# Optimization experiments

Measured on AMD Instinct MI355X. Metric: run time of the kernel, lower is better.

## Reference

```python
import jax, jax.numpy as jnp
import numpy as np

N_NODES, N_EDGES, N_INC = 50000, 10000, 800000
IN_C, HID_C, OUT_C = 128, 128, 128
EPS = 1e-5  # BatchNorm1d default


def setup_inputs() -> dict:
    key = jax.random.key(0)
    ks = jax.random.split(key, 6)
    x = jax.random.normal(ks[0], (N_NODES, IN_C), jnp.float32)
    node_idx = jax.random.randint(ks[1], (N_INC,), 0, N_NODES)
    edge_idx = jax.random.randint(ks[2], (N_INC,), 0, N_EDGES)
    hyperedge_index = jnp.stack([node_idx, edge_idx])  # [2, nnz]
    hyperedge_weight = jnp.ones((N_EDGES,), jnp.float32)
    s1 = 1.0 / np.sqrt(IN_C)
    s2 = 1.0 / np.sqrt(HID_C)
    W1 = jax.random.uniform(ks[3], (HID_C, IN_C), jnp.float32, -s1, s1)
    b1 = jnp.zeros((HID_C,), jnp.float32)
    gamma = jnp.ones((HID_C,), jnp.float32)
    beta = jnp.zeros((HID_C,), jnp.float32)
    W2 = jax.random.uniform(ks[4], (OUT_C, HID_C), jnp.float32, -s2, s2)
    b2 = jnp.zeros((OUT_C,), jnp.float32)
    return dict(x=x, hyperedge_index=hyperedge_index, hyperedge_weight=hyperedge_weight,
                W1=W1, b1=b1, gamma=gamma, beta=beta, W2=W2, b2=b2)


def _hconv(x, W, b, node_idx, edge_idx, hw):
    """PyG HypergraphConv (heads=1, no attention): D^-1 H B^-1 H^T (X W^T) + b."""
    x = x @ W.T  # [N, out_c]; lin has bias=False in PyG
    # node degrees weighted by hyperedge weight
    D = jax.ops.segment_sum(hw[edge_idx], node_idx, num_segments=N_NODES)
    Dinv = jnp.where(D > 0, 1.0 / D, 0.0)
    # hyperedge degrees
    Bdeg = jax.ops.segment_sum(jnp.ones_like(edge_idx, dtype=x.dtype), edge_idx,
                               num_segments=N_EDGES)
    Binv = jnp.where(Bdeg > 0, 1.0 / Bdeg, 0.0)
    # node -> hyperedge: e_e = B_e^-1 * sum_{i in e} x_i
    e = jax.ops.segment_sum(Binv[edge_idx][:, None] * x[node_idx], edge_idx,
                            num_segments=N_EDGES)
    # hyperedge -> node: out_i = D_i^-1 * sum_{e ni i} e_e
    out = jax.ops.segment_sum(Dinv[node_idx][:, None] * e[edge_idx], node_idx,
                              num_segments=N_NODES)
    return out + b  # PyG adds bias after propagation


def reference(x, hyperedge_index, hyperedge_weight, W1, b1, gamma, beta, W2, b2):
    node_idx, edge_idx = hyperedge_index[0], hyperedge_index[1]
    h = _hconv(x, W1, b1, node_idx, edge_idx, hyperedge_weight)
    # BatchNorm1d (training mode: batch statistics, biased variance)
    mu = h.mean(axis=0)
    var = h.var(axis=0)
    h = gamma * (h - mu) * jax.lax.rsqrt(var + EPS) + beta
    return _hconv(h, W2, b2, node_idx, edge_idx, hyperedge_weight)
```

## Files before the change

### kernel.cpp

```cpp
#include <hip/hip_runtime.h>

#define NN 50000
#define NE 10000
#define NI 800000
#define CH 128
#define EPSV 1e-5f
#define ESTR 160
#define NSTR 64
#define NPART 8
#define FCHUNK 2000
#define EPB 8

__global__ __launch_bounds__(256) void k_fill_part(const int* __restrict__ nidx,
    const int* __restrict__ eidx, int* __restrict__ cnt_e,
    int* __restrict__ cnt_n, unsigned short* __restrict__ ell_e,
    unsigned short* __restrict__ ell_n) {
  const int part = blockIdx.x & (NPART - 1);
  const int i0 = (blockIdx.x >> 3) * FCHUNK;
  const int e_lo = part * (NE / NPART), e_hi = e_lo + NE / NPART;
  const int n_lo = part * (NN / NPART), n_hi = n_lo + NN / NPART;
  for (int i = i0 + threadIdx.x; i < i0 + FCHUNK; i += 256) {
    int n = nidx[i], e = eidx[i];
    if (e >= e_lo && e < e_hi) {
      int ce = atomicAdd(&cnt_e[e], 1);
      if (ce < ESTR) ell_e[(long)e * ESTR + ce] = (unsigned short)n;
    }
    if (n >= n_lo && n < n_hi) {
      int cn = atomicAdd(&cnt_n[n], 1);
      if (cn < NSTR) ell_n[(long)n * NSTR + cn] = (unsigned short)e;
    }
  }
}

__global__ __launch_bounds__(256) void k_edge_gemm(const int* __restrict__ cnt_e,
    const unsigned short* __restrict__ ell_e, const float* __restrict__ X,
    const float* __restrict__ W, float* __restrict__ Eout,
    const float* __restrict__ scale, const float* __restrict__ shift) {
  __shared__ float As[EPB][132];
  const int tid = threadIdx.x;
  const int e0 = blockIdx.x * EPB;
  const int lane = tid & 31, grp = tid >> 5;
  const int c = lane * 4;

  const int e = e0 + grp;
  int t = (e < NE) ? cnt_e[e] : 0;
  if (t > ESTR) t = ESTR;
  const unsigned short* base = ell_e + (long)e * ESTR;
  float4 acc = make_float4(0.f, 0.f, 0.f, 0.f);
  int j = 0;
  for (; j + 8 <= t; j += 8) {
    ushort4 na = *reinterpret_cast<const ushort4*>(base + j);
    ushort4 nb = *reinterpret_cast<const ushort4*>(base + j + 4);
    float4 v0 = *reinterpret_cast<const float4*>(&X[(long)na.x * CH + c]);
    float4 v1 = *reinterpret_cast<const float4*>(&X[(long)na.y * CH + c]);
    float4 v2 = *reinterpret_cast<const float4*>(&X[(long)na.z * CH + c]);
    float4 v3 = *reinterpret_cast<const float4*>(&X[(long)na.w * CH + c]);
    float4 v4 = *reinterpret_cast<const float4*>(&X[(long)nb.x * CH + c]);
    float4 v5 = *reinterpret_cast<const float4*>(&X[(long)nb.y * CH + c]);
    float4 v6 = *reinterpret_cast<const float4*>(&X[(long)nb.z * CH + c]);
    float4 v7 = *reinterpret_cast<const float4*>(&X[(long)nb.w * CH + c]);
    acc.x += ((v0.x + v1.x) + (v2.x + v3.x)) + ((v4.x + v5.x) + (v6.x + v7.x));
    acc.y += ((v0.y + v1.y) + (v2.y + v3.y)) + ((v4.y + v5.y) + (v6.y + v7.y));
    acc.z += ((v0.z + v1.z) + (v2.z + v3.z)) + ((v4.z + v5.z) + (v6.z + v7.z));
    acc.w += ((v0.w + v1.w) + (v2.w + v3.w)) + ((v4.w + v5.w) + (v6.w + v7.w));
  }
  for (; j + 4 <= t; j += 4) {
    ushort4 na = *reinterpret_cast<const ushort4*>(base + j);
    float4 v0 = *reinterpret_cast<const float4*>(&X[(long)na.x * CH + c]);
    float4 v1 = *reinterpret_cast<const float4*>(&X[(long)na.y * CH + c]);
    float4 v2 = *reinterpret_cast<const float4*>(&X[(long)na.z * CH + c]);
    float4 v3 = *reinterpret_cast<const float4*>(&X[(long)na.w * CH + c]);
    acc.x += (v0.x + v1.x) + (v2.x + v3.x);
    acc.y += (v0.y + v1.y) + (v2.y + v3.y);
    acc.z += (v0.z + v1.z) + (v2.z + v3.z);
    acc.w += (v0.w + v1.w) + (v2.w + v3.w);
  }
  for (; j < t; ++j) {
    int n = base[j];
    float4 v = *reinterpret_cast<const float4*>(&X[(long)n * CH + c]);
    acc.x += v.x; acc.y += v.y; acc.z += v.z; acc.w += v.w;
  }
  float binv = (t > 0) ? 1.f / (float)t : 0.f;
  float4 m = make_float4(acc.x * binv, acc.y * binv, acc.z * binv, acc.w * binv);
  if (scale) {
    m.x = scale[c + 0] * m.x + shift[c + 0];
    m.y = scale[c + 1] * m.y + shift[c + 1];
    m.z = scale[c + 2] * m.z + shift[c + 2];
    m.w = scale[c + 3] * m.w + shift[c + 3];
  }
  As[grp][c + 0] = m.x; As[grp][c + 1] = m.y;
  As[grp][c + 2] = m.z; As[grp][c + 3] = m.w;
  __syncthreads();

  float a0 = 0.f, a1 = 0.f, a2 = 0.f, a3 = 0.f;
  #pragma unroll 4
  for (int kq = 0; kq < 32; ++kq) {
    float4 a = *reinterpret_cast<const float4*>(&As[grp][kq * 4]);
    float4 w0 = *reinterpret_cast<const float4*>(&W[(long)(c + 0) * CH + kq * 4]);
    float4 w1 = *reinterpret_cast<const float4*>(&W[(long)(c + 1) * CH + kq * 4]);
    float4 w2 = *reinterpret_cast<const float4*>(&W[(long)(c + 2) * CH + kq * 4]);
    float4 w3 = *reinterpret_cast<const float4*>(&W[(long)(c + 3) * CH + kq * 4]);
    a0 += a.x * w0.x + a.y * w0.y + a.z * w0.z + a.w * w0.w;
    a1 += a.x * w1.x + a.y * w1.y + a.z * w1.z + a.w * w1.w;
    a2 += a.x * w2.x + a.y * w2.y + a.z * w2.z + a.w * w2.w;
    a3 += a.x * w3.x + a.y * w3.y + a.z * w3.z + a.w * w3.w;
  }
  if (e < NE) {
    float4 o = make_float4(a0, a1, a2, a3);
    *reinterpret_cast<float4*>(&Eout[(long)e * CH + c]) = o;
  }
}

__global__ __launch_bounds__(256) void k_gather_node(const int* __restrict__ cnt_n,
    const unsigned short* __restrict__ ell_n, const float* __restrict__ hw,
    const float* __restrict__ Eacc, const float* __restrict__ bias,
    float* __restrict__ Out) {
  int gid = blockIdx.x * 256 + threadIdx.x;
  int i = gid >> 5;
  if (i >= NN) return;
  int c = (gid & 31) * 4;
  const float4 bb = *reinterpret_cast<const float4*>(&bias[c]);
  int t = cnt_n[i];
  if (t > NSTR) t = NSTR;
  const unsigned short* base = ell_n + (long)i * NSTR;
  float4 acc = make_float4(0.f, 0.f, 0.f, 0.f);
  float wsum = 0.f;
  int j = 0;
  for (; j + 8 <= t; j += 8) {
    ushort4 ea = *reinterpret_cast<const ushort4*>(base + j);
    ushort4 eb = *reinterpret_cast<const ushort4*>(base + j + 4);
    wsum += ((hw[ea.x] + hw[ea.y]) + (hw[ea.z] + hw[ea.w])) +
            ((hw[eb.x] + hw[eb.y]) + (hw[eb.z] + hw[eb.w]));
    float4 v0 = *reinterpret_cast<const float4*>(&Eacc[(long)ea.x * CH + c]);
    float4 v1 = *reinterpret_cast<const float4*>(&Eacc[(long)ea.y * CH + c]);
    float4 v2 = *reinterpret_cast<const float4*>(&Eacc[(long)ea.z * CH + c]);
    float4 v3 = *reinterpret_cast<const float4*>(&Eacc[(long)ea.w * CH + c]);
    float4 v4 = *reinterpret_cast<const float4*>(&Eacc[(long)eb.x * CH + c]);
    float4 v5 = *reinterpret_cast<const float4*>(&Eacc[(long)eb.y * CH + c]);
    float4 v6 = *reinterpret_cast<const float4*>(&Eacc[(long)eb.z * CH + c]);
    float4 v7 = *reinterpret_cast<const float4*>(&Eacc[(long)eb.w * CH + c]);
    acc.x += ((v0.x + v1.x) + (v2.x + v3.x)) + ((v4.x + v5.x) + (v6.x + v7.x));
    acc.y += ((v0.y + v1.y) + (v2.y + v3.y)) + ((v4.y + v5.y) + (v6.y + v7.y));
    acc.z += ((v0.z + v1.z) + (v2.z + v3.z)) + ((v4.z + v5.z) + (v6.z + v7.z));
    acc.w += ((v0.w + v1.w) + (v2.w + v3.w)) + ((v4.w + v5.w) + (v6.w + v7.w));
  }
  for (; j + 4 <= t; j += 4) {
    ushort4 ea = *reinterpret_cast<const ushort4*>(base + j);
    wsum += (hw[ea.x] + hw[ea.y]) + (hw[ea.z] + hw[ea.w]);
    float4 v0 = *reinterpret_cast<const float4*>(&Eacc[(long)ea.x * CH + c]);
    float4 v1 = *reinterpret_cast<const float4*>(&Eacc[(long)ea.y * CH + c]);
    float4 v2 = *reinterpret_cast<const float4*>(&Eacc[(long)ea.z * CH + c]);
    float4 v3 = *reinterpret_cast<const float4*>(&Eacc[(long)ea.w * CH + c]);
    acc.x += (v0.x + v1.x) + (v2.x + v3.x);
    acc.y += (v0.y + v1.y) + (v2.y + v3.y);
    acc.z += (v0.z + v1.z) + (v2.z + v3.z);
    acc.w += (v0.w + v1.w) + (v2.w + v3.w);
  }
  for (; j < t; ++j) {
    int ee = base[j];
    wsum += hw[ee];
    float4 v = *reinterpret_cast<const float4*>(&Eacc[(long)ee * CH + c]);
    acc.x += v.x; acc.y += v.y; acc.z += v.z; acc.w += v.w;
  }
  float dinv = wsum > 0.f ? 1.f / wsum : 0.f;
  float4 o;
  o.x = dinv * acc.x + bb.x; o.y = dinv * acc.y + bb.y;
  o.z = dinv * acc.z + bb.z; o.w = dinv * acc.w + bb.w;
  *reinterpret_cast<float4*>(&Out[(long)i * CH + c]) = o;
}

__global__ __launch_bounds__(256) void k_colstats(const float* __restrict__ H,
    float* __restrict__ colsum, float* __restrict__ colsq) {
  const int tid = threadIdx.x;
  const int cp = (tid & 63) * 2;
  const int rh = tid >> 6;
  float s0 = 0, s1 = 0, q0 = 0, q1 = 0;
  for (int r = blockIdx.x * 4 + rh; r < NN; r += gridDim.x * 4) {
    float2 v = *reinterpret_cast<const float2*>(&H[(long)r * CH + cp]);
    s0 += v.x; s1 += v.y; q0 += v.x * v.x; q1 += v.y * v.y;
  }
  __shared__ float sh[256][4];
  sh[tid][0] = s0; sh[tid][1] = s1; sh[tid][2] = q0; sh[tid][3] = q1;
  __syncthreads();
  if (tid < 64) {
    float ts0 = 0, ts1 = 0, tq0 = 0, tq1 = 0;
    #pragma unroll
    for (int g = 0; g < 4; ++g) {
      ts0 += sh[tid + g * 64][0]; ts1 += sh[tid + g * 64][1];
      tq0 += sh[tid + g * 64][2]; tq1 += sh[tid + g * 64][3];
    }
    atomicAdd(&colsum[cp], ts0); atomicAdd(&colsum[cp + 1], ts1);
    atomicAdd(&colsq[cp], tq0);  atomicAdd(&colsq[cp + 1], tq1);
  }
}

__global__ void k_bn_params(const float* __restrict__ colsum,
    const float* __restrict__ colsq, const float* __restrict__ gamma,
    const float* __restrict__ beta, float* __restrict__ scl,
    float* __restrict__ shf) {
  int c = threadIdx.x;
  if (c >= CH) return;
  float mu = colsum[c] * (1.f / NN);
  float var = colsq[c] * (1.f / NN) - mu * mu;
  float a = gamma[c] * rsqrtf(var + EPSV);
  scl[c] = a;
  shf[c] = beta[c] - mu * a;
}

extern "C" void kernel_launch(void* const* d_in, const int* in_sizes, int n_in,
                              void* d_out, int out_size, void* d_ws, size_t ws_size,
                              hipStream_t stream) {
  const float* x     = (const float*)d_in[0];
  const int*   hidx  = (const int*)d_in[1];
  const float* hw    = (const float*)d_in[2];
  const float* W1    = (const float*)d_in[3];
  const float* b1    = (const float*)d_in[4];
  const float* gamma = (const float*)d_in[5];
  const float* beta  = (const float*)d_in[6];
  const float* W2    = (const float*)d_in[7];
  const float* b2    = (const float*)d_in[8];
  float* out = (float*)d_out;

  const int* nidx = hidx;
  const int* eidx = hidx + NI;

  char* wb = (char*)d_ws;
  int* cnt_e = (int*)wb;
  int* cnt_n = cnt_e + NE;
  unsigned short* ell_e = (unsigned short*)(cnt_n + NN);
  unsigned short* ell_n = ell_e + (long)NE * ESTR;
  size_t bytes = (size_t)(NE + NN) * 4 + ((size_t)NE * ESTR + (size_t)NN * NSTR) * 2;
  bytes = (bytes + 15) & ~(size_t)15;
  float* wf = (float*)(wb + bytes);
  float* colsum = wf;
  float* colsq  = wf + 128;
  float* scl    = wf + 256;
  float* shf    = wf + 384;
  float* Eacc   = wf + 512;
  float* H      = out;

  hipMemsetAsync(cnt_e, 0, (size_t)(NE + NN) * sizeof(int), stream);
  hipMemsetAsync(colsum, 0, 256 * sizeof(float), stream);
  k_fill_part<<<(NI / FCHUNK) * NPART, 256, 0, stream>>>(nidx, eidx, cnt_e, cnt_n,
                                                         ell_e, ell_n);

  k_edge_gemm<<<NE / EPB, 256, 0, stream>>>(cnt_e, ell_e, x, W1, Eacc,
                                            nullptr, nullptr);
  k_gather_node<<<(NN * 32 + 255) / 256, 256, 0, stream>>>(cnt_n, ell_n, hw,
                                                           Eacc, b1, H);
  k_colstats<<<512, 256, 0, stream>>>(H, colsum, colsq);
  k_bn_params<<<1, 128, 0, stream>>>(colsum, colsq, gamma, beta, scl, shf);

  k_edge_gemm<<<NE / EPB, 256, 0, stream>>>(cnt_e, ell_e, H, W2, Eacc,
                                            scl, shf);
  k_gather_node<<<(NN * 32 + 255) / 256, 256, 0, stream>>>(cnt_n, ell_n, hw,
                                                           Eacc, b2, out);
}
```

Baseline: 509.2 us.

## Split hyperedge gather into node-partitioned fp16 partial sums reduced in GEMM kernel

Hyperedge incidence lists are split into 8 partitions by node index modulo 8, so each partial-gather block reads a narrower node subset and there are more blocks to spread the gather. Partial sums are stored as packed fp16 with nontemporal stores, and a new GEMM kernel reduces the 8 partials before applying W. This is meant to improve cache locality and parallelism of the gather, at the cost of an extra kernel launch, extra partial-sum traffic and fp16 rounding of the partials. The per-partition capacity of 32 and the smaller node stride of 48 could truncate lists for skewed inputs.

```diff
diff --git a/kernel.cpp b/kernel.cpp
--- a/kernel.cpp
+++ b/kernel.cpp
@@ -1,29 +1,32 @@
 #include <hip/hip_runtime.h>
+#include <hip/hip_fp16.h>
 
 #define NN 50000
 #define NE 10000
 #define NI 800000
 #define CH 128
 #define EPSV 1e-5f
-#define ESTR 160
-#define NSTR 64
 #define NPART 8
+#define ESTRP 32
+#define NSTR 48
 #define FCHUNK 2000
-#define EPB 8
-
-__global__ __launch_bounds__(256) void k_fill_part(const int* __restrict__ nidx,
-    const int* __restrict__ eidx, int* __restrict__ cnt_e,
-    int* __restrict__ cnt_n, unsigned short* __restrict__ ell_e,
+
+typedef unsigned long long u64;
+union H2U { __half2 h; unsigned u; };
+
+__global__ __launch_bounds__(256) void k_fill2(const int* __restrict__ nidx,
+    const int* __restrict__ eidx, int* __restrict__ cnt_ep,
+    int* __restrict__ cnt_n, unsigned short* __restrict__ ell_ep,
     unsigned short* __restrict__ ell_n) {
-  const int part = blockIdx.x & (NPART - 1);
+  const int q = blockIdx.x & (NPART - 1);
   const int i0 = (blockIdx.x >> 3) * FCHUNK;
-  const int e_lo = part * (NE / NPART), e_hi = e_lo + NE / NPART;
-  const int n_lo = part * (NN / NPART), n_hi = n_lo + NN / NPART;
+  const int n_lo = q * (NN / NPART), n_hi = n_lo + NN / NPART;
   for (int i = i0 + threadIdx.x; i < i0 + FCHUNK; i += 256) {
     int n = nidx[i], e = eidx[i];
-    if (e >= e_lo && e < e_hi) {
-      int ce = atomicAdd(&cnt_e[e], 1);
-      if (ce < ESTR) ell_e[(long)e * ESTR + ce] = (unsigned short)n;
+    if ((n & 7) == q) {
+      int idx = q * NE + e;
+      int ce = atomicAdd(&cnt_ep[idx], 1);
+      if (ce < ESTRP) ell_ep[(long)idx * ESTRP + ce] = (unsigned short)n;
     }
     if (n >= n_lo && n < n_hi) {
       int cn = atomicAdd(&cnt_n[n], 1);
@@ -32,44 +35,25 @@
   }
 }
 
-__global__ __launch_bounds__(256) void k_edge_gemm(const int* __restrict__ cnt_e,
-    const unsigned short* __restrict__ ell_e, const float* __restrict__ X,
-    const float* __restrict__ W, float* __restrict__ Eout,
-    const float* __restrict__ scale, const float* __restrict__ shift) {
-  __shared__ float As[EPB][132];
-  const int tid = threadIdx.x;
-  const int e0 = blockIdx.x * EPB;
-  const int lane = tid & 31, grp = tid >> 5;
+__global__ __launch_bounds__(256) void k_partial(const int* __restrict__ cnt_ep,
+    const unsigned short* __restrict__ ell_ep, const float* __restrict__ X,
+    u64* __restrict__ Pacc) {
+  const int p = blockIdx.x & (NPART - 1);
+  const int g = threadIdx.x >> 5, lane = threadIdx.x & 31;
+  const int e = (blockIdx.x >> 3) * 8 + g;
   const int c = lane * 4;
-
-  const int e = e0 + grp;
-  int t = (e < NE) ? cnt_e[e] : 0;
-  if (t > ESTR) t = ESTR;
-  const unsigned short* base = ell_e + (long)e * ESTR;
+  const int idx = p * NE + e;
+  int t = cnt_ep[idx];
+  if (t > ESTRP) t = ESTRP;
+  const unsigned short* base = ell_ep + (long)idx * ESTRP;
   float4 acc = make_float4(0.f, 0.f, 0.f, 0.f);
   int j = 0;
-  for (; j + 8 <= t; j += 8) {
-    ushort4 na = *reinterpret_cast<const ushort4*>(base + j);
-    ushort4 nb = *reinterpret_cast<const ushort4*>(base + j + 4);
-    float4 v0 = *reinterpret_cast<const float4*>(&X[(long)na.x * CH + c]);
-    float4 v1 = *reinterpret_cast<const float4*>(&X[(long)na.y * CH + c]);
-    float4 v2 = *reinterpret_cast<const float4*>(&X[(long)na.z * CH + c]);
-    float4 v3 = *reinterpret_cast<const float4*>(&X[(long)na.w * CH + c]);
-    float4 v4 = *reinterpret_cast<const float4*>(&X[(long)nb.x * CH + c]);
-    float4 v5 = *reinterpret_cast<const float4*>(&X[(long)nb.y * CH + c]);
-    float4 v6 = *reinterpret_cast<const float4*>(&X[(long)nb.z * CH + c]);
-    float4 v7 = *reinterpret_cast<const float4*>(&X[(long)nb.w * CH + c]);
-    acc.x += ((v0.x + v1.x) + (v2.x + v3.x)) + ((v4.x + v5.x) + (v6.x + v7.x));
-    acc.y += ((v0.y + v1.y) + (v2.y + v3.y)) + ((v4.y + v5.y) + (v6.y + v7.y));
-    acc.z += ((v0.z + v1.z) + (v2.z + v3.z)) + ((v4.z + v5.z) + (v6.z + v7.z));
-    acc.w += ((v0.w + v1.w) + (v2.w + v3.w)) + ((v4.w + v5.w) + (v6.w + v7.w));
-  }
   for (; j + 4 <= t; j += 4) {
-    ushort4 na = *reinterpret_cast<const ushort4*>(base + j);
-    float4 v0 = *reinterpret_cast<const float4*>(&X[(long)na.x * CH + c]);
-    float4 v1 = *reinterpret_cast<const float4*>(&X[(long)na.y * CH + c]);
-    float4 v2 = *reinterpret_cast<const float4*>(&X[(long)na.z * CH + c]);
-    float4 v3 = *reinterpret_cast<const float4*>(&X[(long)na.w * CH + c]);
+    ushort4 nn = *reinterpret_cast<const ushort4*>(base + j);
+    float4 v0 = *reinterpret_cast<const float4*>(&X[(long)nn.x * CH + c]);
+    float4 v1 = *reinterpret_cast<const float4*>(&X[(long)nn.y * CH + c]);
+    float4 v2 = *reinterpret_cast<const float4*>(&X[(long)nn.z * CH + c]);
+    float4 v3 = *reinterpret_cast<const float4*>(&X[(long)nn.w * CH + c]);
     acc.x += (v0.x + v1.x) + (v2.x + v3.x);
     acc.y += (v0.y + v1.y) + (v2.y + v3.y);
     acc.z += (v0.z + v1.z) + (v2.z + v3.z);
@@ -79,6 +63,35 @@
     int n = base[j];
     float4 v = *reinterpret_cast<const float4*>(&X[(long)n * CH + c]);
     acc.x += v.x; acc.y += v.y; acc.z += v.z; acc.w += v.w;
+  }
+  H2U a, b;
+  a.h = __floats2half2_rn(acc.x, acc.y);
+  b.h = __floats2half2_rn(acc.z, acc.w);
+  u64 pk = ((u64)b.u << 32) | (u64)a.u;
+  __builtin_nontemporal_store(pk, &Pacc[((long)idx * CH + c) >> 2]);
+}
+
+__global__ __launch_bounds__(256) void k_edge_gemm2(const int* __restrict__ cnt_ep,
+    const u64* __restrict__ Pacc, const float* __restrict__ W,
+    float* __restrict__ Eacc, const float* __restrict__ scale,
+    const float* __restrict__ shift) {
+  __shared__ float As[8][132];
+  const int g = threadIdx.x >> 5, lane = threadIdx.x & 31;
+  const int e = blockIdx.x * 8 + g;
+  const int c = lane * 4;
+
+  float4 acc = make_float4(0.f, 0.f, 0.f, 0.f);
+  int t = 0;
+  #pragma unroll
+  for (int p = 0; p < NPART; ++p) {
+    t += cnt_ep[p * NE + e];
+    u64 pk = Pacc[((long)(p * NE + e) * CH + c) >> 2];
+    H2U a, b;
+    a.u = (unsigned)pk;
+    b.u = (unsigned)(pk >> 32);
+    float2 f01 = __half22float2(a.h);
+    float2 f23 = __half22float2(b.h);
+    acc.x += f01.x; acc.y += f01.y; acc.z += f23.x; acc.w += f23.y;
   }
   float binv = (t > 0) ? 1.f / (float)t : 0.f;
   float4 m = make_float4(acc.x * binv, acc.y * binv, acc.z * binv, acc.w * binv);
@@ -88,14 +101,14 @@
     m.z = scale[c + 2] * m.z + shift[c + 2];
     m.w = scale[c + 3] * m.w + shift[c + 3];
   }
-  As[grp][c + 0] = m.x; As[grp][c + 1] = m.y;
-  As[grp][c + 2] = m.z; As[grp][c + 3] = m.w;
+  As[g][c + 0] = m.x; As[g][c + 1] = m.y;
+  As[g][c + 2] = m.z; As[g][c + 3] = m.w;
   __syncthreads();
 
   float a0 = 0.f, a1 = 0.f, a2 = 0.f, a3 = 0.f;
   #pragma unroll 4
   for (int kq = 0; kq < 32; ++kq) {
-    float4 a = *reinterpret_cast<const float4*>(&As[grp][kq * 4]);
+    float4 a = *reinterpret_cast<const float4*>(&As[g][kq * 4]);
     float4 w0 = *reinterpret_cast<const float4*>(&W[(long)(c + 0) * CH + kq * 4]);
     float4 w1 = *reinterpret_cast<const float4*>(&W[(long)(c + 1) * CH + kq * 4]);
     float4 w2 = *reinterpret_cast<const float4*>(&W[(long)(c + 2) * CH + kq * 4]);
@@ -105,10 +118,8 @@
     a2 += a.x * w2.x + a.y * w2.y + a.z * w2.z + a.w * w2.w;
     a3 += a.x * w3.x + a.y * w3.y + a.z * w3.z + a.w * w3.w;
   }
-  if (e < NE) {
-    float4 o = make_float4(a0, a1, a2, a3);
-    *reinterpret_cast<float4*>(&Eout[(long)e * CH + c]) = o;
-  }
+  float4 o = make_float4(a0, a1, a2, a3);
+  *reinterpret_cast<float4*>(&Eacc[(long)e * CH + c]) = o;
 }
 
 __global__ __launch_bounds__(256) void k_gather_node(const int* __restrict__ cnt_n,
@@ -225,34 +236,34 @@
   const int* eidx = hidx + NI;
 
   char* wb = (char*)d_ws;
-  int* cnt_e = (int*)wb;
-  int* cnt_n = cnt_e + NE;
-  unsigned short* ell_e = (unsigned short*)(cnt_n + NN);
-  unsigned short* ell_n = ell_e + (long)NE * ESTR;
-  size_t bytes = (size_t)(NE + NN) * 4 + ((size_t)NE * ESTR + (size_t)NN * NSTR) * 2;
-  bytes = (bytes + 15) & ~(size_t)15;
-  float* wf = (float*)(wb + bytes);
+  int* cnt_n  = (int*)wb;
+  int* cnt_ep = cnt_n + NN;
+  unsigned short* ell_ep = (unsigned short*)(cnt_ep + NPART * NE);
+  unsigned short* ell_n  = ell_ep + (long)NPART * NE * ESTRP;
+  u64*   Pacc = (u64*)(ell_n + (long)NN * NSTR);
+  float* Eacc = (float*)(Pacc + (long)NPART * NE * CH / 4);
+  float* wf   = Eacc + (long)NE * CH;
   float* colsum = wf;
   float* colsq  = wf + 128;
   float* scl    = wf + 256;
   float* shf    = wf + 384;
-  float* Eacc   = wf + 512;
   float* H      = out;
 
-  hipMemsetAsync(cnt_e, 0, (size_t)(NE + NN) * sizeof(int), stream);
+  hipMemsetAsync(cnt_n, 0, (size_t)(NN + NPART * NE) * sizeof(int), stream);
   hipMemsetAsync(colsum, 0, 256 * sizeof(float), stream);
-  k_fill_part<<<(NI / FCHUNK) * NPART, 256, 0, stream>>>(nidx, eidx, cnt_e, cnt_n,
-                                                         ell_e, ell_n);
-
-  k_edge_gemm<<<NE / EPB, 256, 0, stream>>>(cnt_e, ell_e, x, W1, Eacc,
-                                            nullptr, nullptr);
+  k_fill2<<<(NI / FCHUNK) * NPART, 256, 0, stream>>>(nidx, eidx, cnt_ep, cnt_n,
+                                                     ell_ep, ell_n);
+
+  k_partial<<<NE, 256, 0, stream>>>(cnt_ep, ell_ep, x, Pacc);
+  k_edge_gemm2<<<NE / 8, 256, 0, stream>>>(cnt_ep, Pacc, W1, Eacc,
+                                           nullptr, nullptr);
   k_gather_node<<<(NN * 32 + 255) / 256, 256, 0, stream>>>(cnt_n, ell_n, hw,
                                                            Eacc, b1, H);
   k_colstats<<<512, 256, 0, stream>>>(H, colsum, colsq);
   k_bn_params<<<1, 128, 0, stream>>>(colsum, colsq, gamma, beta, scl, shf);
 
-  k_edge_gemm<<<NE / EPB, 256, 0, stream>>>(cnt_e, ell_e, H, W2, Eacc,
-                                            scl, shf);
+  k_partial<<<NE, 256, 0, stream>>>(cnt_ep, ell_ep, H, Pacc);
+  k_edge_gemm2<<<NE / 8, 256, 0, stream>>>(cnt_ep, Pacc, W2, Eacc, scl, shf);
   k_gather_node<<<(NN * 32 + 255) / 256, 256, 0, stream>>>(cnt_n, ell_n, hw,
                                                            Eacc, b2, out);
 }
```

Result: faster. 462.9 us (-9.1%).
